# Kernel optimization log

Measured on AMD Instinct MI355X. Metric: run time of the kernel, lower is better.

Reference implementation:

```python
import jax, jax.numpy as jnp
import numpy as np

N, C, H, W = 32, 3, 512, 512
NUM_BANDS = 16


def _band_masks(h, w, num_bands):
    # Replicates torch.bucketize(radii, bin_edges, right=True) - 1 then clamp.
    y, x = np.meshgrid(np.arange(h, dtype=np.float32),
                       np.arange(w, dtype=np.float32), indexing='ij')
    cy, cx = h // 2, w // 2
    radii = np.sqrt((x - cx) ** 2 + (y - cy) ** 2)
    edges = np.linspace(0.0, radii.max(), num_bands + 1).astype(np.float32)
    idx = np.searchsorted(edges, radii.ravel(), side='right') - 1
    idx = np.clip(idx, 0, num_bands - 1).reshape(h, w)
    masks = (idx[None, :, :] == np.arange(num_bands)[:, None, None]).astype(np.float32)
    return jnp.asarray(masks)  # [num_bands, H, W]


def setup_inputs() -> dict:
    key = jax.random.key(0)
    k1, k2, k3 = jax.random.split(key, 3)
    predictions = jax.random.normal(k1, (N, C, H, W), dtype=jnp.float32)
    ground_truths = jax.random.normal(k2, (N, C, H, W), dtype=jnp.float32)
    band_weights = jax.random.uniform(k3, (NUM_BANDS,), dtype=jnp.float32)
    band_masks = _band_masks(H, W, NUM_BANDS)
    return {
        'predictions': predictions,
        'ground_truths': ground_truths,
        'band_weights': band_weights,
        'band_masks': band_masks,
    }


def reference(predictions, ground_truths, band_weights, band_masks):
    # error -> unitary (ortho) FFT2 -> fftshift to match precomputed radial masks
    err = predictions - ground_truths  # [N,C,H,W]
    F = jnp.fft.fftshift(jnp.fft.fft2(err, norm='ortho'), axes=(-2, -1))
    power = F.real ** 2 + F.imag ** 2  # |FFT|^2, [N,C,H,W]
    # Parseval (ortho FFT is unitary): mean(|ifft2(ifftshift(mask*F))|^2)
    # over the full [N,C,H,W] tensor equals sum(mask*|F|^2) / (N*C*H*W).
    band_sums = jnp.einsum('bhw,nchw->b', band_masks, power)  # [num_bands]
    band_mses = band_sums / power.size
    return jnp.sum(band_mses * band_weights)  # scalar weighted loss
```

## Files before the change

### kernel.cpp

```cpp
#include <hip/hip_runtime.h>
#include <math.h>

#define HW 512
#define LOG2HW 9
#define NIMG 96
#define NBANDS 16
#define NCOL 257
#define PSTRIDE 518
#define IMG_U32 (16 * 4096 + 256)
#define TPITCH 72
#define PI_F 3.14159265358979323846f

typedef float v2f __attribute__((ext_vector_type(2)));

__device__ __forceinline__ float2 cadd(float2 a, float2 b){return make_float2(a.x+b.x, a.y+b.y);}
__device__ __forceinline__ float2 csub(float2 a, float2 b){return make_float2(a.x-b.x, a.y-b.y);}
__device__ __forceinline__ float2 cmul(float2 a, float2 b){return make_float2(a.x*b.x - a.y*b.y, a.x*b.y + a.y*b.x);}
__device__ __forceinline__ float2 mul_negi(float2 a){return make_float2(a.y, -a.x);}

__device__ __forceinline__ int dr9(int p) {
    return ((p & 7) << 6) | (p & 56) | ((p >> 6) & 7);
}

__device__ __forceinline__ int swz(int i)  { return i ^ (((i >> 6) & 7) << 2); }

__device__ __forceinline__ void dft8(const float2 u[8], float2 v[8]) {
    const float R = 0.70710678118654752440f;
    float2 s0 = cadd(u[0], u[4]), s1 = cadd(u[2], u[6]);
    float2 d0 = csub(u[0], u[4]), d1 = csub(u[2], u[6]);
    float2 E0 = cadd(s0, s1), E2 = csub(s0, s1);
    float2 ni = mul_negi(d1);
    float2 E1 = cadd(d0, ni), E3 = csub(d0, ni);
    float2 t0 = cadd(u[1], u[5]), t1 = cadd(u[3], u[7]);
    float2 e0 = csub(u[1], u[5]), e1 = csub(u[3], u[7]);
    float2 O0 = cadd(t0, t1), O2 = csub(t0, t1);
    float2 mi = mul_negi(e1);
    float2 O1 = cadd(e0, mi), O3 = csub(e0, mi);
    float2 w1O = make_float2(R * (O1.x + O1.y), R * (O1.y - O1.x));
    float2 w2O = mul_negi(O2);
    float2 w3O = make_float2(R * (O3.y - O3.x), -R * (O3.x + O3.y));
    v[0] = cadd(E0, O0);  v[4] = csub(E0, O0);
    v[1] = cadd(E1, w1O); v[5] = csub(E1, w1O);
    v[2] = cadd(E2, w2O); v[6] = csub(E2, w2O);
    v[3] = cadd(E3, w3O); v[7] = csub(E3, w3O);
}

__device__ __forceinline__ void twiddle_mul8(float2 v[8], float ang) {
    float sn, cs;
    __sincosf(ang, &sn, &cs);
    float2 w1 = make_float2(cs, sn);
    float2 w2 = cmul(w1, w1), w3 = cmul(w2, w1), w4 = cmul(w2, w2);
    float2 w5 = cmul(w3, w2), w6 = cmul(w3, w3), w7 = cmul(w4, w3);
    v[1] = cmul(v[1], w1); v[2] = cmul(v[2], w2); v[3] = cmul(v[3], w3);
    v[4] = cmul(v[4], w4); v[5] = cmul(v[5], w5); v[6] = cmul(v[6], w6);
    v[7] = cmul(v[7], w7);
}

__device__ __forceinline__ void fft512_wave(float2* zz, float2 u[8], float2 v[8], int j) {
    dft8(u, v);
    twiddle_mul8(v, -(2.0f * PI_F / 512.0f) * (float)j);
    #pragma unroll
    for (int s = 0; s < 8; ++s) zz[swz(j + 64 * s)] = v[s];
    __builtin_amdgcn_wave_barrier();
    const int sb = j >> 3, r = j & 7;
    #pragma unroll
    for (int e = 0; e < 8; ++e) u[e] = zz[swz(64 * sb + r + 8 * e)];
    __builtin_amdgcn_wave_barrier();
    dft8(u, v);
    twiddle_mul8(v, -(2.0f * PI_F / 64.0f) * (float)r);
    #pragma unroll
    for (int s = 0; s < 8; ++s) zz[swz(64 * sb + r + 8 * s)] = v[s];
    __builtin_amdgcn_wave_barrier();
    #pragma unroll
    for (int e = 0; e < 8; ++e) u[e] = zz[swz(8 * j + e)];
    __builtin_amdgcn_wave_barrier();
    dft8(u, v);
}

__global__ void wmapk_kernel(const float* __restrict__ bw,
                             const float* __restrict__ masks,
                             float* __restrict__ wmapk) {
    int idx = blockIdx.x * 256 + threadIdx.x;
    int k1 = idx >> LOG2HW, k2 = idx & (HW - 1);
    int p1 = (k1 + HW / 2) & (HW - 1);
    int p2 = (k2 + HW / 2) & (HW - 1);
    int off = p1 * HW + p2;
    float s = 0.f;
    #pragma unroll
    for (int b = 0; b < NBANDS; ++b)
        s += bw[b] * __builtin_nontemporal_load(&masks[b * HW * HW + off]);
    wmapk[idx] = s;
}

__global__ void wfold_kernel(const float* __restrict__ wmapk,
                             float* __restrict__ wfold_dr) {
    int idx = blockIdx.x * 256 + threadIdx.x;
    if (idx >= NCOL * HW) return;
    int c = idx >> LOG2HW, p = idx & (HW - 1);
    int k1 = dr9(p);
    float s = wmapk[k1 * HW + c];
    if (c >= 1 && c <= 255)
        s += wmapk[((HW - k1) & (HW - 1)) * HW + (HW - c)];
    wfold_dr[idx] = s * (1.0f / (512.0f * 512.0f));
}

__global__ __launch_bounds__(512, 4)
void rowfft_kernel(const float* __restrict__ pred,
                   const float* __restrict__ gt,
                   unsigned* __restrict__ fdata, int img0) {
    __shared__ float2 z[8 * PSTRIDE];
    const int limg = blockIdx.y;
    const int t = threadIdx.x;
    const int wv = t >> 6, j = t & 63;
    const int img = img0 + limg;
    const int f = blockIdx.x * 8 + wv;

    float2* zz = z + wv * PSTRIDE;
    const size_t rbase = ((size_t)img * HW + 2 * f) * HW;
    const float4* pA = (const float4*)(pred + rbase);
    const float4* gA = (const float4*)(gt + rbase);
    const float4* pB = (const float4*)(pred + rbase + HW);
    const float4* gB = (const float4*)(gt + rbase + HW);

    #pragma unroll
    for (int it = 0; it < 2; ++it) {
        int c4 = j + 64 * it;
        float4 a = pA[c4], b = gA[c4], d = pB[c4], e4 = gB[c4];
        float4* dst = (float4*)(zz + swz(4 * c4));
        dst[0] = make_float4(a.x - b.x, d.x - e4.x, a.y - b.y, d.y - e4.y);
        dst[1] = make_float4(a.z - b.z, d.z - e4.z, a.w - b.w, d.w - e4.w);
    }
    __builtin_amdgcn_wave_barrier();

    float2 u[8], v[8];
    #pragma unroll
    for (int e = 0; e < 8; ++e) u[e] = zz[swz(j + 64 * e)];
    __builtin_amdgcn_wave_barrier();
    fft512_wave(zz, u, v, j);
    __builtin_amdgcn_wave_barrier();

    const int m = 8 * (j & 7) + (j >> 3);
    #pragma unroll
    for (int s = 0; s < 8; ++s) zz[swz(64 * s + m)] = v[s];
    __syncthreads();

    const int cl = t & 15;
    const int q  = (t >> 4) & 7;
    const int hw = t >> 7;
    const float2* zq = z + q * PSTRIDE;
    unsigned* img_base = fdata + (size_t)limg * IMG_U32;
    const int rpg = blockIdx.x * 8 + q;
    #pragma unroll
    for (int kb = 0; kb < 4; ++kb) {
        int c = kb * 64 + hw * 16 + cl;
        float2 Zc = zq[swz(c)];
        float2 Zn = zq[swz((HW - c) & (HW - 1))];
        float ax = 0.5f * (Zc.x + Zn.x), ay = 0.5f * (Zc.y - Zn.y);
        float bx = 0.5f * (Zc.y + Zn.y), by = 0.5f * (Zn.x - Zc.x);
        int w0 = __builtin_amdgcn_cvt_pk_fp8_f32(ax, ay, 0, false);
        int w1 = __builtin_amdgcn_cvt_pk_fp8_f32(bx, by, w0, true);
        img_base[(kb * 4 + hw) * 4096 + rpg * 16 + cl] = (unsigned)w1;
    }
    if (t < 8) {
        const float2* zq2 = z + t * PSTRIDE;
        float2 Zc = zq2[swz(256)];
        int w0 = __builtin_amdgcn_cvt_pk_fp8_f32(Zc.x, 0.f, 0, false);
        int w1 = __builtin_amdgcn_cvt_pk_fp8_f32(Zc.y, 0.f, w0, true);
        img_base[16 * 4096 + blockIdx.x * 8 + t] = (unsigned)w1;
    }
}

__global__ __launch_bounds__(256)
void colfft_kernel(const unsigned* __restrict__ fdata,
                   const float* __restrict__ wfold_dr,
                   float* __restrict__ partials, int img0) {
    __shared__ char tileb[256 * TPITCH];
    __shared__ float2 scr[4 * PSTRIDE];
    const int limg = blockIdx.y;
    const int ct = blockIdx.x;
    const int t = threadIdx.x;
    const int wv = t >> 6, j = t & 63;
    const unsigned* fimg = fdata + (size_t)limg * IMG_U32;
    float2* zz = scr + wv * PSTRIDE;

    if (ct < 16) {
        const uint2* src = (const uint2*)(fimg + ct * 4096);
        #pragma unroll
        for (int k = 0; k < 8; ++k) {
            int i = t + 256 * k;
            int rp = i >> 3, s8 = i & 7;
            *(uint2*)(tileb + rp * TPITCH + s8 * 8) = src[i];
        }
        __syncthreads();

        #pragma unroll
        for (int pass = 0; pass < 4; ++pass) {
            const int cl = wv + 4 * pass;
            const int c = ct * 16 + cl;
            float2 u[8], v[8];
            #pragma unroll
            for (int e = 0; e < 8; ++e) {
                int r = j + 64 * e;
                unsigned hs = *(const unsigned short*)
                    (tileb + (r >> 1) * TPITCH + cl * 4 + (r & 1) * 2);
                v2f d = __builtin_amdgcn_cvt_pk_f32_fp8((int)hs, false);
                u[e] = make_float2(d.x, d.y);
            }
            fft512_wave(zz, u, v, j);
            const float4* w4 = (const float4*)(wfold_dr + (size_t)c * HW + 8 * j);
            float4 wa = w4[0], wb = w4[1];
            float acc = 0.f;
            acc += (v[0].x*v[0].x + v[0].y*v[0].y) * wa.x;
            acc += (v[1].x*v[1].x + v[1].y*v[1].y) * wa.y;
            acc += (v[2].x*v[2].x + v[2].y*v[2].y) * wa.z;
            acc += (v[3].x*v[3].x + v[3].y*v[3].y) * wa.w;
            acc += (v[4].x*v[4].x + v[4].y*v[4].y) * wb.x;
            acc += (v[5].x*v[5].x + v[5].y*v[5].y) * wb.y;
            acc += (v[6].x*v[6].x + v[6].y*v[6].y) * wb.z;
            acc += (v[7].x*v[7].x + v[7].y*v[7].y) * wb.w;
            #pragma unroll
            for (int off = 32; off > 0; off >>= 1)
                acc += __shfl_down(acc, off, 64);
            if (j == 0)
                partials[(size_t)(img0 + limg) * NCOL + c] = acc;
            __builtin_amdgcn_wave_barrier();
        }
    } else if (wv == 0) {
        const unsigned short* s16 = (const unsigned short*)(fimg + 16 * 4096);
        float2 u[8], v[8];
        #pragma unroll
        for (int e = 0; e < 8; ++e) {
            unsigned hs = s16[j + 64 * e];
            v2f d = __builtin_amdgcn_cvt_pk_f32_fp8((int)hs, false);
            u[e] = make_float2(d.x, d.y);
        }
        fft512_wave(zz, u, v, j);
        const float4* w4 = (const float4*)(wfold_dr + (size_t)256 * HW + 8 * j);
        float4 wa = w4[0], wb = w4[1];
        float acc = 0.f;
        acc += (v[0].x*v[0].x + v[0].y*v[0].y) * wa.x;
        acc += (v[1].x*v[1].x + v[1].y*v[1].y) * wa.y;
        acc += (v[2].x*v[2].x + v[2].y*v[2].y) * wa.z;
        acc += (v[3].x*v[3].x + v[3].y*v[3].y) * wa.w;
        acc += (v[4].x*v[4].x + v[4].y*v[4].y) * wb.x;
        acc += (v[5].x*v[5].x + v[5].y*v[5].y) * wb.y;
        acc += (v[6].x*v[6].x + v[6].y*v[6].y) * wb.z;
        acc += (v[7].x*v[7].x + v[7].y*v[7].y) * wb.w;
        #pragma unroll
        for (int off = 32; off > 0; off >>= 1)
            acc += __shfl_down(acc, off, 64);
        if (j == 0)
            partials[(size_t)(img0 + limg) * NCOL + 256] = acc;
    }
}

__global__ __launch_bounds__(1024)
void final_reduce(const float* __restrict__ partials,
                  float* __restrict__ out) {
    __shared__ float red[1024];
    const int t = threadIdx.x;
    float acc = 0.f;
    const float4* p4 = (const float4*)partials;
    for (int i = t; i < (NIMG * NCOL) / 4; i += 1024) {
        float4 v = p4[i];
        acc += v.x + v.y + v.z + v.w;
    }
    red[t] = acc;
    __syncthreads();
    #pragma unroll
    for (int s = 512; s > 0; s >>= 1) {
        if (t < s) red[t] += red[t + s];
        __syncthreads();
    }
    if (t == 0) out[0] = red[0] * (1.0f / 25165824.0f);
}

extern "C" void kernel_launch(void* const* d_in, const int* in_sizes, int n_in,
                              void* d_out, int out_size, void* d_ws, size_t ws_size,
                              hipStream_t stream) {
    const float* pred  = (const float*)d_in[0];
    const float* gt    = (const float*)d_in[1];
    const float* bw    = (const float*)d_in[2];
    const float* masks = (const float*)d_in[3];
    float* out = (float*)d_out;

    char* ws = (char*)d_ws;
    float* wmapk    = (float*)ws;
    float* wfold_dr = (float*)(ws + (1 << 20));
    float* partials = (float*)(ws + (1 << 20) + (576 << 10));
    unsigned* fdata = (unsigned*)(ws + (2 << 20));
    const size_t fixed = (2 << 20);
    const size_t img_bytes = (size_t)IMG_U32 * 4;

    int chunk = 1;
    if (ws_size > fixed + img_bytes)
        chunk = (int)((ws_size - fixed) / img_bytes);
    if (chunk > NIMG) chunk = NIMG;
    if (chunk < 1) chunk = 1;

    wmapk_kernel<<<(HW * HW) / 256, 256, 0, stream>>>(bw, masks, wmapk);
    wfold_kernel<<<(NCOL * HW + 255) / 256, 256, 0, stream>>>(wmapk, wfold_dr);

    for (int img0 = 0; img0 < NIMG; img0 += chunk) {
        int n = NIMG - img0 < chunk ? NIMG - img0 : chunk;
        rowfft_kernel<<<dim3(HW / 16, n), 512, 0, stream>>>(pred, gt, fdata, img0);
        colfft_kernel<<<dim3(17, n), 256, 0, stream>>>(fdata, wfold_dr, partials, img0);
    }

    final_reduce<<<1, 1024, 0, stream>>>(partials, out);
}
```

Before: 71.44 us.

## Process two row-pair groups per rowfft block with prefetched register loads

Each rowfft block now handles 16 row-pairs in two rounds instead of 8. The second round's pred/gt loads are issued into registers before the first round's FFT, so global latency overlaps compute. Input now loads directly into registers with strided scalar reads instead of float4 loads staged through LDS, which removes one LDS round trip. The block count is halved and launch bounds are relaxed to 2 blocks per CU, so register pressure rises and occupancy may fall.

After: 79.32 us. 11.0% more time.

```diff
diff --git a/kernel.cpp b/kernel.cpp
--- a/kernel.cpp
+++ b/kernel.cpp
@@ -104,7 +104,7 @@
     wfold_dr[idx] = s * (1.0f / (512.0f * 512.0f));
 }
 
-__global__ __launch_bounds__(512, 4)
+__global__ __launch_bounds__(512, 2)
 void rowfft_kernel(const float* __restrict__ pred,
                    const float* __restrict__ gt,
                    unsigned* __restrict__ fdata, int img0) {
@@ -113,60 +113,72 @@
     const int t = threadIdx.x;
     const int wv = t >> 6, j = t & 63;
     const int img = img0 + limg;
-    const int f = blockIdx.x * 8 + wv;
+    const int fbase = blockIdx.x * 16;
 
     float2* zz = z + wv * PSTRIDE;
-    const size_t rbase = ((size_t)img * HW + 2 * f) * HW;
-    const float4* pA = (const float4*)(pred + rbase);
-    const float4* gA = (const float4*)(gt + rbase);
-    const float4* pB = (const float4*)(pred + rbase + HW);
-    const float4* gB = (const float4*)(gt + rbase + HW);
-
-    #pragma unroll
-    for (int it = 0; it < 2; ++it) {
-        int c4 = j + 64 * it;
-        float4 a = pA[c4], b = gA[c4], d = pB[c4], e4 = gB[c4];
-        float4* dst = (float4*)(zz + swz(4 * c4));
-        dst[0] = make_float4(a.x - b.x, d.x - e4.x, a.y - b.y, d.y - e4.y);
-        dst[1] = make_float4(a.z - b.z, d.z - e4.z, a.w - b.w, d.w - e4.w);
-    }
-    __builtin_amdgcn_wave_barrier();
-
-    float2 u[8], v[8];
-    #pragma unroll
-    for (int e = 0; e < 8; ++e) u[e] = zz[swz(j + 64 * e)];
-    __builtin_amdgcn_wave_barrier();
-    fft512_wave(zz, u, v, j);
-    __builtin_amdgcn_wave_barrier();
-
-    const int m = 8 * (j & 7) + (j >> 3);
-    #pragma unroll
-    for (int s = 0; s < 8; ++s) zz[swz(64 * s + m)] = v[s];
-    __syncthreads();
-
-    const int cl = t & 15;
-    const int q  = (t >> 4) & 7;
-    const int hw = t >> 7;
-    const float2* zq = z + q * PSTRIDE;
     unsigned* img_base = fdata + (size_t)limg * IMG_U32;
-    const int rpg = blockIdx.x * 8 + q;
-    #pragma unroll
-    for (int kb = 0; kb < 4; ++kb) {
-        int c = kb * 64 + hw * 16 + cl;
-        float2 Zc = zq[swz(c)];
-        float2 Zn = zq[swz((HW - c) & (HW - 1))];
-        float ax = 0.5f * (Zc.x + Zn.x), ay = 0.5f * (Zc.y - Zn.y);
-        float bx = 0.5f * (Zc.y + Zn.y), by = 0.5f * (Zn.x - Zc.x);
-        int w0 = __builtin_amdgcn_cvt_pk_fp8_f32(ax, ay, 0, false);
-        int w1 = __builtin_amdgcn_cvt_pk_fp8_f32(bx, by, w0, true);
-        img_base[(kb * 4 + hw) * 4096 + rpg * 16 + cl] = (unsigned)w1;
-    }
-    if (t < 8) {
-        const float2* zq2 = z + t * PSTRIDE;
-        float2 Zc = zq2[swz(256)];
-        int w0 = __builtin_amdgcn_cvt_pk_fp8_f32(Zc.x, 0.f, 0, false);
-        int w1 = __builtin_amdgcn_cvt_pk_fp8_f32(Zc.y, 0.f, w0, true);
-        img_base[16 * 4096 + blockIdx.x * 8 + t] = (unsigned)w1;
+    const size_t ibase = (size_t)img * HW * HW;
+
+    float a0[8], a1[8], b0[8], b1[8];
+    {
+        const float* pa = pred + ibase + (size_t)(2 * (fbase + wv)) * HW + j;
+        const float* ga = gt   + ibase + (size_t)(2 * (fbase + wv)) * HW + j;
+        #pragma unroll
+        for (int e = 0; e < 8; ++e) {
+            a0[e] = pa[64 * e];  a1[e] = pa[HW + 64 * e];
+            b0[e] = ga[64 * e];  b1[e] = ga[HW + 64 * e];
+        }
+    }
+
+    #pragma unroll
+    for (int round = 0; round < 2; ++round) {
+        float2 u[8], v[8];
+        #pragma unroll
+        for (int e = 0; e < 8; ++e)
+            u[e] = make_float2(a0[e] - b0[e], a1[e] - b1[e]);
+
+        if (round == 0) {
+            const float* pa = pred + ibase + (size_t)(2 * (fbase + 8 + wv)) * HW + j;
+            const float* ga = gt   + ibase + (size_t)(2 * (fbase + 8 + wv)) * HW + j;
+            #pragma unroll
+            for (int e = 0; e < 8; ++e) {
+                a0[e] = pa[64 * e];  a1[e] = pa[HW + 64 * e];
+                b0[e] = ga[64 * e];  b1[e] = ga[HW + 64 * e];
+            }
+        }
+
+        fft512_wave(zz, u, v, j);
+        __builtin_amdgcn_wave_barrier();
+
+        const int m = 8 * (j & 7) + (j >> 3);
+        #pragma unroll
+        for (int s = 0; s < 8; ++s) zz[swz(64 * s + m)] = v[s];
+        __syncthreads();
+
+        const int cl = t & 15;
+        const int q  = (t >> 4) & 7;
+        const int hw = t >> 7;
+        const float2* zq = z + q * PSTRIDE;
+        const int rpg = fbase + round * 8 + q;
+        #pragma unroll
+        for (int kb = 0; kb < 4; ++kb) {
+            int c = kb * 64 + hw * 16 + cl;
+            float2 Zc = zq[swz(c)];
+            float2 Zn = zq[swz((HW - c) & (HW - 1))];
+            float ax = 0.5f * (Zc.x + Zn.x), ay = 0.5f * (Zc.y - Zn.y);
+            float bx = 0.5f * (Zc.y + Zn.y), by = 0.5f * (Zn.x - Zc.x);
+            int w0 = __builtin_amdgcn_cvt_pk_fp8_f32(ax, ay, 0, false);
+            int w1 = __builtin_amdgcn_cvt_pk_fp8_f32(bx, by, w0, true);
+            img_base[(kb * 4 + hw) * 4096 + rpg * 16 + cl] = (unsigned)w1;
+        }
+        if (t < 8) {
+            const float2* zq2 = z + t * PSTRIDE;
+            float2 Zc = zq2[swz(256)];
+            int w0 = __builtin_amdgcn_cvt_pk_fp8_f32(Zc.x, 0.f, 0, false);
+            int w1 = __builtin_amdgcn_cvt_pk_fp8_f32(Zc.y, 0.f, w0, true);
+            img_base[16 * 4096 + fbase + round * 8 + t] = (unsigned)w1;
+        }
+        if (round == 0) __syncthreads();
     }
 }
 
@@ -303,7 +315,7 @@
 
     for (int img0 = 0; img0 < NIMG; img0 += chunk) {
         int n = NIMG - img0 < chunk ? NIMG - img0 : chunk;
-        rowfft_kernel<<<dim3(HW / 16, n), 512, 0, stream>>>(pred, gt, fdata, img0);
+        rowfft_kernel<<<dim3(16, n), 512, 0, stream>>>(pred, gt, fdata, img0);
         colfft_kernel<<<dim3(17, n), 256, 0, stream>>>(fdata, wfold_dr, partials, img0);
     }
 
```

## Pipeline row FFT with async global-to-LDS loads, 8 row-pairs per wave

Applied to the files above, without the earlier changes.

The row FFT kernel now has each wave process 8 row pairs in sequence. It prefetches the next pair's pred and gt rows straight into LDS with global_load_lds while it runs the current FFT, and uses manual vmcnt waits. The intermediate fp8 layout changes to a row-major [row-pair][column] u32 array, and the column kernel transposes it through a padded 17-pitch LDS tile. The aim is to hide global load latency and drop the block-wide sync, at the cost of fewer blocks (8 per image) and lower parallelism.

Result: slower. 75.40 us (+5.5%).

```diff
diff --git a/kernel.cpp b/kernel.cpp
--- a/kernel.cpp
+++ b/kernel.cpp
@@ -1,5 +1,6 @@
 #include <hip/hip_runtime.h>
 #include <math.h>
+#include <stdint.h>
 
 #define HW 512
 #define LOG2HW 9
@@ -7,11 +8,20 @@
 #define NBANDS 16
 #define NCOL 257
 #define PSTRIDE 518
-#define IMG_U32 (16 * 4096 + 256)
-#define TPITCH 72
+#define NP 8
+#define IMG_U32 (256 * 256 + 256)
 #define PI_F 3.14159265358979323846f
 
 typedef float v2f __attribute__((ext_vector_type(2)));
+typedef __attribute__((address_space(1))) const unsigned gas_u32;
+typedef __attribute__((address_space(3))) unsigned las_u32;
+
+__device__ __forceinline__ void gll16(const float* g, const float* l) {
+    gas_u32* gp = reinterpret_cast<gas_u32*>(reinterpret_cast<uintptr_t>(g));
+    las_u32* lp = reinterpret_cast<las_u32*>(
+        (unsigned)reinterpret_cast<uintptr_t>(l));
+    __builtin_amdgcn_global_load_lds(gp, lp, 16, 0, 0);
+}
 
 __device__ __forceinline__ float2 cadd(float2 a, float2 b){return make_float2(a.x+b.x, a.y+b.y);}
 __device__ __forceinline__ float2 csub(float2 a, float2 b){return make_float2(a.x-b.x, a.y-b.y);}
@@ -21,7 +31,6 @@
 __device__ __forceinline__ int dr9(int p) {
     return ((p & 7) << 6) | (p & 56) | ((p >> 6) & 7);
 }
-
 __device__ __forceinline__ int swz(int i)  { return i ^ (((i >> 6) & 7) << 2); }
 
 __device__ __forceinline__ void dft8(const float2 u[8], float2 v[8]) {
@@ -104,69 +113,81 @@
     wfold_dr[idx] = s * (1.0f / (512.0f * 512.0f));
 }
 
-__global__ __launch_bounds__(512, 4)
+__device__ __forceinline__ void stage_pack(const float* pbase, const float* gbase,
+                                           int pf, float* stg, int j) {
+    const float* pr = pbase + (size_t)(2 * pf) * HW;
+    const float* gr = gbase + (size_t)(2 * pf) * HW;
+    #pragma unroll
+    for (int ch = 0; ch < 4; ++ch)
+        gll16(pr + 256 * ch + 4 * j, stg + 256 * ch);
+    #pragma unroll
+    for (int ch = 0; ch < 4; ++ch)
+        gll16(gr + 256 * ch + 4 * j, stg + 1024 + 256 * ch);
+}
+
+__global__ __launch_bounds__(256)
 void rowfft_kernel(const float* __restrict__ pred,
                    const float* __restrict__ gt,
                    unsigned* __restrict__ fdata, int img0) {
-    __shared__ float2 z[8 * PSTRIDE];
+    __shared__ float2 scr[4 * PSTRIDE];
+    __shared__ float stage[4 * 2048];
     const int limg = blockIdx.y;
     const int t = threadIdx.x;
     const int wv = t >> 6, j = t & 63;
     const int img = img0 + limg;
-    const int f = blockIdx.x * 8 + wv;
-
-    float2* zz = z + wv * PSTRIDE;
-    const size_t rbase = ((size_t)img * HW + 2 * f) * HW;
-    const float4* pA = (const float4*)(pred + rbase);
-    const float4* gA = (const float4*)(gt + rbase);
-    const float4* pB = (const float4*)(pred + rbase + HW);
-    const float4* gB = (const float4*)(gt + rbase + HW);
-
-    #pragma unroll
-    for (int it = 0; it < 2; ++it) {
-        int c4 = j + 64 * it;
-        float4 a = pA[c4], b = gA[c4], d = pB[c4], e4 = gB[c4];
-        float4* dst = (float4*)(zz + swz(4 * c4));
-        dst[0] = make_float4(a.x - b.x, d.x - e4.x, a.y - b.y, d.y - e4.y);
-        dst[1] = make_float4(a.z - b.z, d.z - e4.z, a.w - b.w, d.w - e4.w);
-    }
-    __builtin_amdgcn_wave_barrier();
-
-    float2 u[8], v[8];
-    #pragma unroll
-    for (int e = 0; e < 8; ++e) u[e] = zz[swz(j + 64 * e)];
-    __builtin_amdgcn_wave_barrier();
-    fft512_wave(zz, u, v, j);
-    __builtin_amdgcn_wave_barrier();
-
-    const int m = 8 * (j & 7) + (j >> 3);
-    #pragma unroll
-    for (int s = 0; s < 8; ++s) zz[swz(64 * s + m)] = v[s];
-    __syncthreads();
-
-    const int cl = t & 15;
-    const int q  = (t >> 4) & 7;
-    const int hw = t >> 7;
-    const float2* zq = z + q * PSTRIDE;
-    unsigned* img_base = fdata + (size_t)limg * IMG_U32;
-    const int rpg = blockIdx.x * 8 + q;
-    #pragma unroll
-    for (int kb = 0; kb < 4; ++kb) {
-        int c = kb * 64 + hw * 16 + cl;
-        float2 Zc = zq[swz(c)];
-        float2 Zn = zq[swz((HW - c) & (HW - 1))];
-        float ax = 0.5f * (Zc.x + Zn.x), ay = 0.5f * (Zc.y - Zn.y);
-        float bx = 0.5f * (Zc.y + Zn.y), by = 0.5f * (Zn.x - Zc.x);
-        int w0 = __builtin_amdgcn_cvt_pk_fp8_f32(ax, ay, 0, false);
-        int w1 = __builtin_amdgcn_cvt_pk_fp8_f32(bx, by, w0, true);
-        img_base[(kb * 4 + hw) * 4096 + rpg * 16 + cl] = (unsigned)w1;
-    }
-    if (t < 8) {
-        const float2* zq2 = z + t * PSTRIDE;
-        float2 Zc = zq2[swz(256)];
-        int w0 = __builtin_amdgcn_cvt_pk_fp8_f32(Zc.x, 0.f, 0, false);
-        int w1 = __builtin_amdgcn_cvt_pk_fp8_f32(Zc.y, 0.f, w0, true);
-        img_base[16 * 4096 + blockIdx.x * 8 + t] = (unsigned)w1;
+    const int f0 = (blockIdx.x * 4 + wv) * NP;
+
+    float2* zz = scr + wv * PSTRIDE;
+    float* stg = stage + wv * 2048;
+    unsigned* img_fd = fdata + (size_t)limg * IMG_U32;
+    const float* pbase = pred + (size_t)img * HW * HW;
+    const float* gbase = gt + (size_t)img * HW * HW;
+
+    stage_pack(pbase, gbase, f0, stg, j);
+
+    #pragma unroll
+    for (int p = 0; p < NP; ++p) {
+        const int f = f0 + p;
+        if (p == 0) asm volatile("s_waitcnt vmcnt(0)" ::: "memory");
+        else        asm volatile("s_waitcnt vmcnt(5)" ::: "memory");
+
+        float2 u[8], v[8];
+        #pragma unroll
+        for (int e = 0; e < 8; ++e) {
+            int i = j + 64 * e;
+            u[e] = make_float2(stg[i] - stg[1024 + i],
+                               stg[512 + i] - stg[1536 + i]);
+        }
+        asm volatile("s_waitcnt lgkmcnt(0)" ::: "memory");
+        if (p < NP - 1)
+            stage_pack(pbase, gbase, f + 1, stg, j);
+
+        fft512_wave(zz, u, v, j);
+        __builtin_amdgcn_wave_barrier();
+
+        const int m = 8 * (j & 7) + (j >> 3);
+        #pragma unroll
+        for (int s = 0; s < 8; ++s) zz[swz(64 * s + m)] = v[s];
+        __builtin_amdgcn_wave_barrier();
+
+        #pragma unroll
+        for (int i = 0; i < 4; ++i) {
+            int c = j + 64 * i;
+            float2 Zc = zz[swz(c)];
+            float2 Zn = zz[swz((HW - c) & (HW - 1))];
+            float ax = 0.5f * (Zc.x + Zn.x), ay = 0.5f * (Zc.y - Zn.y);
+            float bx = 0.5f * (Zc.y + Zn.y), by = 0.5f * (Zn.x - Zc.x);
+            int w0 = __builtin_amdgcn_cvt_pk_fp8_f32(ax, ay, 0, false);
+            int w1 = __builtin_amdgcn_cvt_pk_fp8_f32(bx, by, w0, true);
+            img_fd[f * 256 + c] = (unsigned)w1;
+        }
+        if (j == 0) {
+            float2 Zc = zz[swz(256)];
+            int w0 = __builtin_amdgcn_cvt_pk_fp8_f32(Zc.x, 0.f, 0, false);
+            int w1 = __builtin_amdgcn_cvt_pk_fp8_f32(Zc.y, 0.f, w0, true);
+            img_fd[65536 + f] = (unsigned)w1;
+        }
+        __builtin_amdgcn_wave_barrier();
     }
 }
 
@@ -174,36 +195,34 @@
 void colfft_kernel(const unsigned* __restrict__ fdata,
                    const float* __restrict__ wfold_dr,
                    float* __restrict__ partials, int img0) {
-    __shared__ char tileb[256 * TPITCH];
+    __shared__ unsigned tile32[256 * 17];
     __shared__ float2 scr[4 * PSTRIDE];
     const int limg = blockIdx.y;
-    const int ct = blockIdx.x;
+    const int cb = blockIdx.x;
     const int t = threadIdx.x;
     const int wv = t >> 6, j = t & 63;
     const unsigned* fimg = fdata + (size_t)limg * IMG_U32;
     float2* zz = scr + wv * PSTRIDE;
 
-    if (ct < 16) {
-        const uint2* src = (const uint2*)(fimg + ct * 4096);
-        #pragma unroll
-        for (int k = 0; k < 8; ++k) {
-            int i = t + 256 * k;
-            int rp = i >> 3, s8 = i & 7;
-            *(uint2*)(tileb + rp * TPITCH + s8 * 8) = src[i];
+    if (cb < 16) {
+        const int c0 = cb * 16;
+        #pragma unroll
+        for (int k = 0; k < 16; ++k) {
+            int f = (t >> 4) + 16 * k, cl = t & 15;
+            tile32[f * 17 + cl] = fimg[f * 256 + c0 + cl];
         }
         __syncthreads();
 
         #pragma unroll
         for (int pass = 0; pass < 4; ++pass) {
             const int cl = wv + 4 * pass;
-            const int c = ct * 16 + cl;
+            const int c = c0 + cl;
             float2 u[8], v[8];
             #pragma unroll
             for (int e = 0; e < 8; ++e) {
                 int r = j + 64 * e;
-                unsigned hs = *(const unsigned short*)
-                    (tileb + (r >> 1) * TPITCH + cl * 4 + (r & 1) * 2);
-                v2f d = __builtin_amdgcn_cvt_pk_f32_fp8((int)hs, false);
+                unsigned w32 = tile32[(r >> 1) * 17 + cl] >> (16 * (r & 1));
+                v2f d = __builtin_amdgcn_cvt_pk_f32_fp8((int)w32, false);
                 u[e] = make_float2(d.x, d.y);
             }
             fft512_wave(zz, u, v, j);
@@ -226,12 +245,13 @@
             __builtin_amdgcn_wave_barrier();
         }
     } else if (wv == 0) {
-        const unsigned short* s16 = (const unsigned short*)(fimg + 16 * 4096);
+        const unsigned* tail = fimg + 65536;
         float2 u[8], v[8];
         #pragma unroll
         for (int e = 0; e < 8; ++e) {
-            unsigned hs = s16[j + 64 * e];
-            v2f d = __builtin_amdgcn_cvt_pk_f32_fp8((int)hs, false);
+            int r = j + 64 * e;
+            unsigned w32 = tail[r >> 1] >> (16 * (r & 1));
+            v2f d = __builtin_amdgcn_cvt_pk_f32_fp8((int)w32, false);
             u[e] = make_float2(d.x, d.y);
         }
         fft512_wave(zz, u, v, j);
@@ -303,7 +323,7 @@
 
     for (int img0 = 0; img0 < NIMG; img0 += chunk) {
         int n = NIMG - img0 < chunk ? NIMG - img0 : chunk;
-        rowfft_kernel<<<dim3(HW / 16, n), 512, 0, stream>>>(pred, gt, fdata, img0);
+        rowfft_kernel<<<dim3(8, n), 256, 0, stream>>>(pred, gt, fdata, img0);
         colfft_kernel<<<dim3(17, n), 256, 0, stream>>>(fdata, wfold_dr, partials, img0);
     }
 
```
